# Performance work log

Hardware: AMD Instinct MI355X
Metric: run time of the kernel (lower is better)

## Reference

```python
import jax, jax.numpy as jnp
import numpy as np

B, R, C, NH = 8, 64, 256, 8
N = R * R            # 4096 tokens
HD = C // NH         # head dim 32
FF = 3               # focusing factor

def dwconv(x, w, b):
    # x: (B, C, H, W); w: (C, 1, kh, kw) depthwise
    y = jax.lax.conv_general_dilated(
        x, w, window_strides=(1, 1), padding='SAME',
        dimension_numbers=('NCHW', 'OIHW', 'NCHW'),
        feature_group_count=x.shape[1])
    return y + b[None, :, None, None]

def setup_inputs() -> dict:
    key = jax.random.key(0)
    ks = jax.random.split(key, 6)
    return {
        'qkv': jax.random.normal(ks[0], (3, B, N, C), jnp.float32),
        'pos_enc': jax.random.normal(ks[1], (1, N, C), jnp.float32) * 0.02,
        'scale': jax.random.normal(ks[2], (1, 1, C), jnp.float32) * 0.02,
        'w_v': jax.random.normal(ks[3], (C, 1, 3, 3), jnp.float32) * 0.1,
        'b_v': jnp.zeros((C,), jnp.float32),
        'w_dwc': jax.random.normal(ks[4], (HD, 1, 5, 5), jnp.float32) * 0.1,
        'b_dwc': jnp.zeros((HD,), jnp.float32),
    }

def reference(qkv, pos_enc, scale, w_v, b_v, w_dwc, b_dwc):
    q, k, v = qkv[0], qkv[1], qkv[2]          # each (B, N, C)
    # --- LePE: depthwise 3x3 conv on v over full channel dim ---
    v_img = v.transpose(0, 2, 1).reshape(B, C, R, R)
    lepe = dwconv(v_img, w_v, b_v)            # (B, C, R, R)
    lepe = lepe.reshape(B * NH, HD, N).transpose(0, 2, 1)   # (B*h, N, hd)
    v = v_img.reshape(B, C, N).transpose(0, 2, 1)           # (B, N, C)
    # --- focused kernelization ---
    k = k + pos_enc
    sc = jax.nn.softplus(scale)
    q = (jax.nn.relu(q) + 1e-6) / sc
    k = (jax.nn.relu(k) + 1e-6) / sc
    qn = jnp.linalg.norm(q, axis=-1, keepdims=True)
    kn = jnp.linalg.norm(k, axis=-1, keepdims=True)
    q = q ** FF
    k = k ** FF
    q = q / jnp.linalg.norm(q, axis=-1, keepdims=True) * qn
    k = k / jnp.linalg.norm(k, axis=-1, keepdims=True) * kn
    split = lambda x: x.reshape(B, N, NH, HD).transpose(0, 2, 1, 3).reshape(B * NH, N, HD)
    q, k, v = split(q), split(k), split(v)    # (B*h, N, hd)
    # --- linear attention (kv aggregation path: N >> hd) ---
    z = 1.0 / (jnp.einsum('bic,bc->bi', q, k.sum(axis=1)) + 1e-6)
    kv = jnp.einsum('bjc,bjd->bcd', k, v)     # (B*h, hd, hd)
    x = jnp.einsum('bic,bcd,bi->bid', q, kv, z)
    # --- dwc feature mixing on v per head ---
    fm = v.transpose(0, 2, 1).reshape(B * NH, HD, R, R)
    fm = dwconv(fm, w_dwc, b_dwc).reshape(B * NH, HD, N).transpose(0, 2, 1)
    x = x + fm + lepe
    x = x.reshape(B, NH, N, HD).transpose(0, 2, 1, 3).reshape(B, N, C)
    return x
```

## Files before the change

kernel.cpp:

```cpp
#include <hip/hip_runtime.h>
#include <math.h>

#define B_  8
#define R_  64
#define C_  256
#define NH_ 8
#define N_  4096
#define HD_ 32

__global__ __launch_bounds__(256) void kernelA(
        const float* __restrict__ qkv, const float* __restrict__ pos,
        const float* __restrict__ scale,
        float* __restrict__ qf, float* __restrict__ kf) {
    const int t    = threadIdx.x;
    const int wave = t >> 6, lane = t & 63;
    const int tok  = blockIdx.x * 4 + wave;
    const int b    = tok >> 12;
    const int n    = tok & (N_ - 1);
    const int c0   = lane * 4;

    const size_t qidx = ((size_t)(b * N_ + n)) * C_ + c0;
    const float4 q4 = *(const float4*)(qkv + qidx);
    const float4 k4 = *(const float4*)(qkv + (size_t)B_ * N_ * C_ + qidx);
    const float4 p4 = *(const float4*)(pos + (size_t)n * C_ + c0);
    const float4 s4 = *(const float4*)(scale + c0);

    float qa[4] = {q4.x, q4.y, q4.z, q4.w};
    float kk[4] = {k4.x, k4.y, k4.z, k4.w};
    float pa[4] = {p4.x, p4.y, p4.z, p4.w};
    float sa[4] = {s4.x, s4.y, s4.z, s4.w};

    float q3[4], k3[4];
    float sq2 = 0.f, sq6 = 0.f, sk2 = 0.f, sk6 = 0.f;
    #pragma unroll
    for (int i = 0; i < 4; i++) {
        const float sc = log1pf(expf(sa[i]));
        float qv = (fmaxf(qa[i], 0.f) + 1e-6f) / sc;
        float kv = (fmaxf(kk[i] + pa[i], 0.f) + 1e-6f) / sc;
        sq2 += qv * qv;  sk2 += kv * kv;
        const float q3v = qv * qv * qv;
        const float k3v = kv * kv * kv;
        q3[i] = q3v;  k3[i] = k3v;
        sq6 += q3v * q3v;  sk6 += k3v * k3v;
    }
    #pragma unroll
    for (int m = 1; m < 64; m <<= 1) {
        sq2 += __shfl_xor(sq2, m, 64);
        sq6 += __shfl_xor(sq6, m, 64);
        sk2 += __shfl_xor(sk2, m, 64);
        sk6 += __shfl_xor(sk6, m, 64);
    }
    const float qs = sqrtf(sq2) * rsqrtf(sq6);
    const float ks = sqrtf(sk2) * rsqrtf(sk6);

    const int h = c0 >> 5, d = c0 & 31;
    const size_t ob = (size_t)b * N_ * C_ + (size_t)h * N_ * HD_
                    + (size_t)n * HD_ + d;
    *(float4*)(qf + ob) = make_float4(q3[0]*qs, q3[1]*qs, q3[2]*qs, q3[3]*qs);
    *(float4*)(kf + ob) = make_float4(k3[0]*ks, k3[1]*ks, k3[2]*ks, k3[3]*ks);
}

__global__ __launch_bounds__(256) void kernelB(
        const float* __restrict__ kf, const float* __restrict__ qkv,
        float* __restrict__ kv_ws, float* __restrict__ ksum_ws) {
    __shared__ float k_s[128 * HD_];
    __shared__ float v_s[128 * HD_];
    const int t     = threadIdx.x;
    const int bh    = blockIdx.x >> 3;
    const int chunk = blockIdx.x & 7;
    const int b     = bh >> 3, h = bh & 7;
    const int c     = t >> 3, p = t & 7, dbase = p * 4;

    float a0 = 0.f, a1 = 0.f, a2 = 0.f, a3 = 0.f, ksp = 0.f;
    const size_t vbase = (size_t)2 * B_ * N_ * C_ + (size_t)b * N_ * C_ + h * HD_;

    for (int tile = 0; tile < 4; tile++) {
        const int n0 = chunk * 512 + tile * 128;
        const float4* ksrc = (const float4*)(kf + (size_t)bh * N_ * HD_ + (size_t)n0 * HD_);
        #pragma unroll
        for (int i = 0; i < 4; i++)
            ((float4*)k_s)[i * 256 + t] = ksrc[i * 256 + t];
        #pragma unroll
        for (int i = 0; i < 4; i++) {
            const int j  = (i * 256 + t) * 4;
            const int nl = j >> 5, d = j & 31;
            ((float4*)v_s)[i * 256 + t] =
                *(const float4*)(qkv + vbase + (size_t)(n0 + nl) * C_ + d);
        }
        __syncthreads();
        #pragma unroll 4
        for (int nl = 0; nl < 128; nl++) {
            const float  kc = k_s[nl * HD_ + c];
            const float4 vv = *(const float4*)&v_s[nl * HD_ + dbase];
            a0 = fmaf(kc, vv.x, a0);
            a1 = fmaf(kc, vv.y, a1);
            a2 = fmaf(kc, vv.z, a2);
            a3 = fmaf(kc, vv.w, a3);
        }
        #pragma unroll
        for (int i = 0; i < 16; i++)
            ksp += k_s[(p + i * 8) * HD_ + c];
        __syncthreads();
    }
    float* kvdst = kv_ws + (size_t)bh * 1024 + c * HD_ + dbase;
    atomicAdd(kvdst + 0, a0);
    atomicAdd(kvdst + 1, a1);
    atomicAdd(kvdst + 2, a2);
    atomicAdd(kvdst + 3, a3);
    k_s[c * 8 + p] = ksp;
    __syncthreads();
    if (t < 32) {
        float s = 0.f;
        #pragma unroll
        for (int i = 0; i < 8; i++) s += k_s[t * 8 + i];
        atomicAdd(&ksum_ws[bh * HD_ + t], s);
    }
}

__global__ __launch_bounds__(256) void kernelCD(
        const float* __restrict__ qkv, const float* __restrict__ qf,
        const float* __restrict__ kv_ws, const float* __restrict__ ksum_ws,
        const float* __restrict__ w_v,  const float* __restrict__ b_v,
        const float* __restrict__ w_dwc, const float* __restrict__ b_dwc,
        float* __restrict__ out) {
    __shared__ float v_s[20 * 20 * 32];
    __shared__ float kv_s[1024];
    __shared__ float ks_s[32];
    const int t    = threadIdx.x;
    const int tile = blockIdx.x;
    const int h    = blockIdx.y;
    const int b    = blockIdx.z;
    const int ty0  = (tile >> 2) * 16, tx0 = (tile & 3) * 16;
    const int bh   = b * NH_ + h;

    ((float4*)kv_s)[t] = ((const float4*)(kv_ws + (size_t)bh * 1024))[t];
    if (t < 32) ks_s[t] = ksum_ws[bh * HD_ + t];

    const float* vb = qkv + (size_t)2 * B_ * N_ * C_ + (size_t)b * N_ * C_ + h * HD_;
    #pragma unroll
    for (int i = 0; i < 13; i++) {
        const int idx = i * 256 + t;
        if (idx < 3200) {
            const int pix = idx >> 3, d4 = (idx & 7) * 4;
            const int yy = pix / 20, xx = pix - yy * 20;
            const int gy = ty0 + yy - 2, gx = tx0 + xx - 2;
            float4 val = make_float4(0.f, 0.f, 0.f, 0.f);
            if (gy >= 0 && gy < R_ && gx >= 0 && gx < R_)
                val = *(const float4*)(vb + (size_t)(gy * R_ + gx) * C_ + d4);
            *(float4*)&v_s[pix * 32 + d4] = val;
        }
    }

    const int c  = t & 31, pg = t >> 5;
    float wv[9], wd[25];
    {
        const float* wvp = w_v + (size_t)(h * HD_ + c) * 9;
        const float* wdp = w_dwc + (size_t)c * 25;
        #pragma unroll
        for (int i = 0; i < 9; i++)  wv[i] = wvp[i];
        #pragma unroll
        for (int i = 0; i < 25; i++) wd[i] = wdp[i];
    }
    const float bias = b_v[h * HD_ + c] + b_dwc[c];
    __syncthreads();

    float res[32];
    #pragma unroll
    for (int r2 = 0; r2 < 2; r2++) {
        const int ty = pg * 2 + r2;
        float win[5][5];
        #pragma unroll
        for (int j = 0; j < 5; j++)
            #pragma unroll
            for (int i = 0; i < 5; i++)
                win[j][i] = v_s[((ty + i) * 20 + j) * 32 + c];
        #pragma unroll
        for (int tx = 0; tx < 16; tx++) {
            float a = bias;
            #pragma unroll
            for (int j = 0; j < 5; j++) {
                const int slot = (tx + j) % 5;
                #pragma unroll
                for (int i = 0; i < 5; i++)
                    a = fmaf(wd[i * 5 + j], win[slot][i], a);
            }
            #pragma unroll
            for (int j = 1; j < 4; j++) {
                const int slot = (tx + j) % 5;
                #pragma unroll
                for (int i = 1; i < 4; i++)
                    a = fmaf(wv[(i - 1) * 3 + (j - 1)], win[slot][i], a);
            }
            res[r2 * 16 + tx] = a;
            if (tx < 15) {
                const int slot = tx % 5;
                #pragma unroll
                for (int i = 0; i < 5; i++)
                    win[slot][i] = v_s[((ty + i) * 20 + (tx + 5)) * 32 + c];
            }
        }
    }
    __syncthreads();
    #pragma unroll
    for (int r2 = 0; r2 < 2; r2++)
        #pragma unroll
        for (int tx = 0; tx < 16; tx++)
            v_s[((pg * 2 + r2) * 16 + tx) * 33 + c] = res[r2 * 16 + tx];
    __syncthreads();

    {
        const int tyy = t >> 4, txx = t & 15;
        const int n   = (ty0 + tyy) * R_ + (tx0 + txx);
        float q[32];
        const float4* qsrc = (const float4*)(qf + (size_t)bh * N_ * HD_ + (size_t)n * HD_);
        #pragma unroll
        for (int i = 0; i < 8; i++) ((float4*)q)[i] = qsrc[i];

        float denom = 1e-6f;
        #pragma unroll
        for (int cc = 0; cc < 32; cc++) denom = fmaf(q[cc], ks_s[cc], denom);
        const float z = 1.f / denom;

        float o[32];
        #pragma unroll
        for (int i = 0; i < 32; i++) o[i] = 0.f;
        #pragma unroll
        for (int cc = 0; cc < 32; cc++) {
            const float qc = q[cc];
            #pragma unroll
            for (int d = 0; d < 32; d++)
                o[d] = fmaf(qc, kv_s[cc * 32 + d], o[d]);
        }
        float* dst = out + ((size_t)(b * N_ + n)) * C_ + h * HD_;
        #pragma unroll
        for (int i = 0; i < 8; i++) {
            float4 v4;
            v4.x = fmaf(o[i*4+0], z, v_s[t * 33 + i*4+0]);
            v4.y = fmaf(o[i*4+1], z, v_s[t * 33 + i*4+1]);
            v4.z = fmaf(o[i*4+2], z, v_s[t * 33 + i*4+2]);
            v4.w = fmaf(o[i*4+3], z, v_s[t * 33 + i*4+3]);
            ((float4*)dst)[i] = v4;
        }
    }
}

extern "C" void kernel_launch(void* const* d_in, const int* in_sizes, int n_in,
                              void* d_out, int out_size, void* d_ws, size_t ws_size,
                              hipStream_t stream) {
    const float* qkv   = (const float*)d_in[0];
    const float* pos   = (const float*)d_in[1];
    const float* scale = (const float*)d_in[2];
    const float* w_v   = (const float*)d_in[3];
    const float* b_v   = (const float*)d_in[4];
    const float* w_dwc = (const float*)d_in[5];
    const float* b_dwc = (const float*)d_in[6];
    float* out = (float*)d_out;

    float* qf      = (float*)d_ws;
    float* kf      = qf + (size_t)B_ * N_ * C_;
    float* kv_ws   = kf + (size_t)B_ * N_ * C_;
    float* ksum_ws = kv_ws + 64 * 1024;

    hipMemsetAsync(kv_ws, 0, (64 * 1024 + 64 * 32) * sizeof(float), stream);
    kernelA<<<dim3(B_ * N_ / 4), 256, 0, stream>>>(qkv, pos, scale, qf, kf);
    kernelB<<<dim3(512), 256, 0, stream>>>(kf, qkv, kv_ws, ksum_ws);
    kernelCD<<<dim3(16, NH_, B_), 256, 0, stream>>>(qkv, qf, kv_ws, ksum_ws,
                                                    w_v, b_v, w_dwc, b_dwc, out);
}
```

Baseline: 234.9 us.

## Store per-token norm scales only and recompute focused q/k in consumers

The first kernel no longer writes full transformed q and k tensors. It writes only one scalar normalization factor per token for q and for k. The kv-aggregation and output kernels re-read raw q/k (and pos) from the input and recompute the relu, scale and cube transform on the fly. This removes two full-size intermediate writes and reads in exchange for extra recomputation and an extra pos read. It also uses fast exp/log intrinsics and nontemporal output stores.

```diff
diff --git a/kernel.cpp b/kernel.cpp
--- a/kernel.cpp
+++ b/kernel.cpp
@@ -8,40 +8,42 @@
 #define N_  4096
 #define HD_ 32
 
-__global__ __launch_bounds__(256) void kernelA(
+typedef float fvec4 __attribute__((ext_vector_type(4)));
+
+__device__ __forceinline__ float softplus_rcp(float s) {
+    return 1.f / __logf(1.f + __expf(s));
+}
+
+__global__ __launch_bounds__(256) void kernelN(
         const float* __restrict__ qkv, const float* __restrict__ pos,
         const float* __restrict__ scale,
-        float* __restrict__ qf, float* __restrict__ kf) {
+        float* __restrict__ qs_arr, float* __restrict__ ks_arr) {
     const int t    = threadIdx.x;
     const int wave = t >> 6, lane = t & 63;
     const int tok  = blockIdx.x * 4 + wave;
-    const int b    = tok >> 12;
     const int n    = tok & (N_ - 1);
     const int c0   = lane * 4;
 
-    const size_t qidx = ((size_t)(b * N_ + n)) * C_ + c0;
+    const size_t qidx = (size_t)tok * C_ + c0;
     const float4 q4 = *(const float4*)(qkv + qidx);
     const float4 k4 = *(const float4*)(qkv + (size_t)B_ * N_ * C_ + qidx);
     const float4 p4 = *(const float4*)(pos + (size_t)n * C_ + c0);
     const float4 s4 = *(const float4*)(scale + c0);
 
     float qa[4] = {q4.x, q4.y, q4.z, q4.w};
-    float kk[4] = {k4.x, k4.y, k4.z, k4.w};
+    float ka[4] = {k4.x, k4.y, k4.z, k4.w};
     float pa[4] = {p4.x, p4.y, p4.z, p4.w};
     float sa[4] = {s4.x, s4.y, s4.z, s4.w};
 
-    float q3[4], k3[4];
     float sq2 = 0.f, sq6 = 0.f, sk2 = 0.f, sk6 = 0.f;
     #pragma unroll
     for (int i = 0; i < 4; i++) {
-        const float sc = log1pf(expf(sa[i]));
-        float qv = (fmaxf(qa[i], 0.f) + 1e-6f) / sc;
-        float kv = (fmaxf(kk[i] + pa[i], 0.f) + 1e-6f) / sc;
+        const float rsc = softplus_rcp(sa[i]);
+        const float qv = (fmaxf(qa[i], 0.f) + 1e-6f) * rsc;
+        const float kv = (fmaxf(ka[i] + pa[i], 0.f) + 1e-6f) * rsc;
         sq2 += qv * qv;  sk2 += kv * kv;
-        const float q3v = qv * qv * qv;
-        const float k3v = kv * kv * kv;
-        q3[i] = q3v;  k3[i] = k3v;
-        sq6 += q3v * q3v;  sk6 += k3v * k3v;
+        const float q3 = qv * qv * qv, k3 = kv * kv * kv;
+        sq6 += q3 * q3;  sk6 += k3 * k3;
     }
     #pragma unroll
     for (int m = 1; m < 64; m <<= 1) {
@@ -50,40 +52,52 @@
         sk2 += __shfl_xor(sk2, m, 64);
         sk6 += __shfl_xor(sk6, m, 64);
     }
-    const float qs = sqrtf(sq2) * rsqrtf(sq6);
-    const float ks = sqrtf(sk2) * rsqrtf(sk6);
-
-    const int h = c0 >> 5, d = c0 & 31;
-    const size_t ob = (size_t)b * N_ * C_ + (size_t)h * N_ * HD_
-                    + (size_t)n * HD_ + d;
-    *(float4*)(qf + ob) = make_float4(q3[0]*qs, q3[1]*qs, q3[2]*qs, q3[3]*qs);
-    *(float4*)(kf + ob) = make_float4(k3[0]*ks, k3[1]*ks, k3[2]*ks, k3[3]*ks);
-}
-
-__global__ __launch_bounds__(256) void kernelB(
-        const float* __restrict__ kf, const float* __restrict__ qkv,
+    if (lane == 0) {
+        qs_arr[tok] = sqrtf(sq2) * rsqrtf(sq6);
+        ks_arr[tok] = sqrtf(sk2) * rsqrtf(sk6);
+    }
+}
+
+__global__ __launch_bounds__(256) void kernelB2(
+        const float* __restrict__ qkv, const float* __restrict__ pos,
+        const float* __restrict__ scale, const float* __restrict__ ks_arr,
         float* __restrict__ kv_ws, float* __restrict__ ksum_ws) {
     __shared__ float k_s[128 * HD_];
     __shared__ float v_s[128 * HD_];
+    __shared__ float rsc_s[HD_];
     const int t     = threadIdx.x;
     const int bh    = blockIdx.x >> 3;
     const int chunk = blockIdx.x & 7;
     const int b     = bh >> 3, h = bh & 7;
     const int c     = t >> 3, p = t & 7, dbase = p * 4;
 
+    if (t < HD_) rsc_s[t] = softplus_rcp(scale[h * HD_ + t]);
+    __syncthreads();
+
     float a0 = 0.f, a1 = 0.f, a2 = 0.f, a3 = 0.f, ksp = 0.f;
+    const size_t kbase = (size_t)B_ * N_ * C_ + (size_t)b * N_ * C_ + h * HD_;
     const size_t vbase = (size_t)2 * B_ * N_ * C_ + (size_t)b * N_ * C_ + h * HD_;
+    const int tokbase = b * N_;
 
     for (int tile = 0; tile < 4; tile++) {
         const int n0 = chunk * 512 + tile * 128;
-        const float4* ksrc = (const float4*)(kf + (size_t)bh * N_ * HD_ + (size_t)n0 * HD_);
-        #pragma unroll
-        for (int i = 0; i < 4; i++)
-            ((float4*)k_s)[i * 256 + t] = ksrc[i * 256 + t];
         #pragma unroll
         for (int i = 0; i < 4; i++) {
             const int j  = (i * 256 + t) * 4;
             const int nl = j >> 5, d = j & 31;
+            const float4 kr = *(const float4*)(qkv + kbase + (size_t)(n0 + nl) * C_ + d);
+            const float4 pr = *(const float4*)(pos + (size_t)(n0 + nl) * C_ + h * HD_ + d);
+            const float ksn = ks_arr[tokbase + n0 + nl];
+            float4 o;
+            {
+                float v0 = (fmaxf(kr.x + pr.x, 0.f) + 1e-6f) * rsc_s[d + 0];
+                float v1 = (fmaxf(kr.y + pr.y, 0.f) + 1e-6f) * rsc_s[d + 1];
+                float v2 = (fmaxf(kr.z + pr.z, 0.f) + 1e-6f) * rsc_s[d + 2];
+                float v3 = (fmaxf(kr.w + pr.w, 0.f) + 1e-6f) * rsc_s[d + 3];
+                o.x = v0 * v0 * v0 * ksn;  o.y = v1 * v1 * v1 * ksn;
+                o.z = v2 * v2 * v2 * ksn;  o.w = v3 * v3 * v3 * ksn;
+            }
+            *(float4*)&k_s[j] = o;
             ((float4*)v_s)[i * 256 + t] =
                 *(const float4*)(qkv + vbase + (size_t)(n0 + nl) * C_ + d);
         }
@@ -117,15 +131,17 @@
     }
 }
 
-__global__ __launch_bounds__(256) void kernelCD(
-        const float* __restrict__ qkv, const float* __restrict__ qf,
+__global__ __launch_bounds__(256) void kernelCD2(
+        const float* __restrict__ qkv, const float* __restrict__ qs_arr,
         const float* __restrict__ kv_ws, const float* __restrict__ ksum_ws,
+        const float* __restrict__ scale,
         const float* __restrict__ w_v,  const float* __restrict__ b_v,
         const float* __restrict__ w_dwc, const float* __restrict__ b_dwc,
         float* __restrict__ out) {
     __shared__ float v_s[20 * 20 * 32];
     __shared__ float kv_s[1024];
     __shared__ float ks_s[32];
+    __shared__ float rsc_s[32];
     const int t    = threadIdx.x;
     const int tile = blockIdx.x;
     const int h    = blockIdx.y;
@@ -134,7 +150,10 @@
     const int bh   = b * NH_ + h;
 
     ((float4*)kv_s)[t] = ((const float4*)(kv_ws + (size_t)bh * 1024))[t];
-    if (t < 32) ks_s[t] = ksum_ws[bh * HD_ + t];
+    if (t < 32) {
+        ks_s[t]  = ksum_ws[bh * HD_ + t];
+        rsc_s[t] = softplus_rcp(scale[h * HD_ + t]);
+    }
 
     const float* vb = qkv + (size_t)2 * B_ * N_ * C_ + (size_t)b * N_ * C_ + h * HD_;
     #pragma unroll
@@ -211,10 +230,17 @@
     {
         const int tyy = t >> 4, txx = t & 15;
         const int n   = (ty0 + tyy) * R_ + (tx0 + txx);
+        const int tok = b * N_ + n;
         float q[32];
-        const float4* qsrc = (const float4*)(qf + (size_t)bh * N_ * HD_ + (size_t)n * HD_);
+        const float4* qsrc = (const float4*)(qkv + (size_t)tok * C_ + h * HD_);
         #pragma unroll
         for (int i = 0; i < 8; i++) ((float4*)q)[i] = qsrc[i];
+        const float qs = qs_arr[tok];
+        #pragma unroll
+        for (int i = 0; i < 32; i++) {
+            const float r = (fmaxf(q[i], 0.f) + 1e-6f) * rsc_s[i];
+            q[i] = r * r * r * qs;
+        }
 
         float denom = 1e-6f;
         #pragma unroll
@@ -231,15 +257,15 @@
             for (int d = 0; d < 32; d++)
                 o[d] = fmaf(qc, kv_s[cc * 32 + d], o[d]);
         }
-        float* dst = out + ((size_t)(b * N_ + n)) * C_ + h * HD_;
+        fvec4* dst = (fvec4*)(out + (size_t)tok * C_ + h * HD_);
         #pragma unroll
         for (int i = 0; i < 8; i++) {
-            float4 v4;
+            fvec4 v4;
             v4.x = fmaf(o[i*4+0], z, v_s[t * 33 + i*4+0]);
             v4.y = fmaf(o[i*4+1], z, v_s[t * 33 + i*4+1]);
             v4.z = fmaf(o[i*4+2], z, v_s[t * 33 + i*4+2]);
             v4.w = fmaf(o[i*4+3], z, v_s[t * 33 + i*4+3]);
-            ((float4*)dst)[i] = v4;
+            __builtin_nontemporal_store(v4, dst + i);
         }
     }
 }
@@ -256,14 +282,14 @@
     const float* b_dwc = (const float*)d_in[6];
     float* out = (float*)d_out;
 
-    float* qf      = (float*)d_ws;
-    float* kf      = qf + (size_t)B_ * N_ * C_;
-    float* kv_ws   = kf + (size_t)B_ * N_ * C_;
+    float* qs_arr  = (float*)d_ws;
+    float* ks_arr  = qs_arr + (size_t)B_ * N_;
+    float* kv_ws   = ks_arr + (size_t)B_ * N_;
     float* ksum_ws = kv_ws + 64 * 1024;
 
-    hipMemsetAsync(kv_ws, 0, (64 * 1024 + 64 * 32) * sizeof(float), stream);
-    kernelA<<<dim3(B_ * N_ / 4), 256, 0, stream>>>(qkv, pos, scale, qf, kf);
-    kernelB<<<dim3(512), 256, 0, stream>>>(kf, qkv, kv_ws, ksum_ws);
-    kernelCD<<<dim3(16, NH_, B_), 256, 0, stream>>>(qkv, qf, kv_ws, ksum_ws,
-                                                    w_v, b_v, w_dwc, b_dwc, out);
-}
+    (void)hipMemsetAsync(kv_ws, 0, (64 * 1024 + 64 * 32) * sizeof(float), stream);
+    kernelN<<<dim3(B_ * N_ / 4), 256, 0, stream>>>(qkv, pos, scale, qs_arr, ks_arr);
+    kernelB2<<<dim3(512), 256, 0, stream>>>(qkv, pos, scale, ks_arr, kv_ws, ksum_ws);
+    kernelCD2<<<dim3(16, NH_, B_), 256, 0, stream>>>(qkv, qs_arr, kv_ws, ksum_ws,
+                                                     scale, w_v, b_v, w_dwc, b_dwc, out);
+}
```

Result: slower. 268.3 us (+14.2%).
